# Performance work log

Measured on AMD Instinct MI355X. Metric: run time of the kernel, lower is better.

Reference implementation:

```python
import jax, jax.numpy as jnp
import numpy as np

IN_F = 4096
OUT_F = 4096
B, S = 4, 2048
RMS_EPS = 1e-6
Q_EPS = 1e-5


def setup_inputs() -> dict:
    key = jax.random.key(0)
    kx, kw, kb, ks = jax.random.split(key, 4)
    x = jax.random.normal(kx, (B, S, IN_F), dtype=jnp.float32)
    # ternary BitNet weight in {-1, 0, +1}, stored as float32 for the reference
    W = (jax.random.randint(kw, (OUT_F, IN_F), 0, 3) - 1).astype(jnp.float32)
    rms_weight = jnp.ones((IN_F,), dtype=jnp.float32)
    bias = jax.random.normal(kb, (OUT_F,), dtype=jnp.float32)
    weight_scale = jax.random.uniform(ks, (1,), dtype=jnp.float32) + 0.5
    return {"x": x, "W": W, "rms_weight": rms_weight, "bias": bias,
            "weight_scale": weight_scale}


def reference(x, W, rms_weight, bias, weight_scale):
    # RMSNorm (self.rms_norm applied before quantized matmul)
    var = jnp.mean(x * x, axis=-1, keepdims=True)
    h = x * jax.lax.rsqrt(var + RMS_EPS) * rms_weight
    # BitNet act_quant: per-token absmax int8 quantization
    scale = 127.0 / jnp.clip(jnp.max(jnp.abs(h), axis=-1, keepdims=True), Q_EPS)  # [B,S,1]
    q = jnp.clip(jnp.round(h * scale), -128.0, 127.0)
    # ternary GEMV per token, then dequant
    y = jnp.einsum('bsk,ok->bso', q, W) / scale  # [B,S,OUT_F]
    y = y + bias
    y = y * weight_scale  # weight_scale_mode == 'multiply'
    return y
```

## Files before the change

### kernel.cpp

```cpp
#include <hip/hip_runtime.h>

#define IN_F 4096
#define OUT_F 4096
#define NTOK 8192
#define KDIM 4096

using i32x4 = __attribute__((ext_vector_type(4))) int;
using f32x4 = __attribute__((ext_vector_type(4))) float;

__device__ __forceinline__ void gload_lds16(const void* g, void* l) {
  __builtin_amdgcn_global_load_lds(
      (const __attribute__((address_space(1))) void*)g,
      (__attribute__((address_space(3))) void*)l, 16, 0, 0);
}

#define WAITV(n) asm volatile("s_waitcnt vmcnt(" #n ")" ::: "memory")
#define BAR() do { asm volatile("" ::: "memory"); __builtin_amdgcn_s_barrier(); \
                   asm volatile("" ::: "memory"); } while (0)

__global__ __launch_bounds__(256) void rmsq_kernel(
    const float* __restrict__ x, const float* __restrict__ rmsw,
    signed char* __restrict__ q, float* __restrict__ dscale) {
  const int tok = blockIdx.x;
  const int tid = threadIdx.x;
  const f32x4* xr = (const f32x4*)(x + (size_t)tok * IN_F);
  const f32x4* wr = (const f32x4*)rmsw;

  f32x4 v[4];
  float ss = 0.f;
#pragma unroll
  for (int c = 0; c < 4; ++c) {
    v[c] = xr[c * 256 + tid];
    ss += v[c].x * v[c].x + v[c].y * v[c].y + v[c].z * v[c].z + v[c].w * v[c].w;
  }

  __shared__ float red[4];
#pragma unroll
  for (int off = 32; off > 0; off >>= 1) ss += __shfl_down(ss, off, 64);
  const int wid = tid >> 6;
  if ((tid & 63) == 0) red[wid] = ss;
  __syncthreads();
  const float tot = red[0] + red[1] + red[2] + red[3];
  const float rinv = rsqrtf(tot * (1.0f / IN_F) + 1e-6f);

  f32x4 h[4];
  float amax = 0.f;
#pragma unroll
  for (int c = 0; c < 4; ++c) {
    f32x4 w = wr[c * 256 + tid];
    h[c].x = v[c].x * rinv * w.x;
    h[c].y = v[c].y * rinv * w.y;
    h[c].z = v[c].z * rinv * w.z;
    h[c].w = v[c].w * rinv * w.w;
    amax = fmaxf(amax, fabsf(h[c].x));
    amax = fmaxf(amax, fabsf(h[c].y));
    amax = fmaxf(amax, fabsf(h[c].z));
    amax = fmaxf(amax, fabsf(h[c].w));
  }

  __syncthreads();
#pragma unroll
  for (int off = 32; off > 0; off >>= 1)
    amax = fmaxf(amax, __shfl_down(amax, off, 64));
  if ((tid & 63) == 0) red[wid] = amax;
  __syncthreads();
  amax = fmaxf(fmaxf(red[0], red[1]), fmaxf(red[2], red[3]));
  amax = fmaxf(amax, 1e-5f);
  const float qs = 127.0f / amax;
  if (tid == 0) dscale[tok] = amax * (1.0f / 127.0f);

  uint* qo = (uint*)(q + (size_t)tok * IN_F);
#pragma unroll
  for (int c = 0; c < 4; ++c) {
    float r0 = fminf(fmaxf(rintf(h[c].x * qs), -128.f), 127.f);
    float r1 = fminf(fmaxf(rintf(h[c].y * qs), -128.f), 127.f);
    float r2 = fminf(fmaxf(rintf(h[c].z * qs), -128.f), 127.f);
    float r3 = fminf(fmaxf(rintf(h[c].w * qs), -128.f), 127.f);
    uint p = ((uint)((int)r0 & 255)) | ((uint)((int)r1 & 255) << 8) |
             ((uint)((int)r2 & 255) << 16) | ((uint)((int)r3 & 255) << 24);
    qo[c * 256 + tid] = p;
  }
}

__global__ __launch_bounds__(256) void wconv_kernel(
    const float* __restrict__ W, signed char* __restrict__ Wq) {
  const int idx = blockIdx.x * 256 + threadIdx.x;
  f32x4 w = ((const f32x4*)W)[idx];
  uint p = ((uint)((int)w.x & 255)) | ((uint)((int)w.y & 255) << 8) |
           ((uint)((int)w.z & 255) << 16) | ((uint)((int)w.w & 255) << 24);
  ((uint*)Wq)[idx] = p;
}

#define BM 256
#define BN 256
#define BK 64
#define NT (KDIM / BK)
#define ABYTES (BM * BK)
#define BUFBYTES (2 * ABYTES)

__global__ __launch_bounds__(512, 2) void gemm_kernel(
    const signed char* __restrict__ A, const signed char* __restrict__ Bw,
    const float* __restrict__ dscale, const float* __restrict__ bias,
    const float* __restrict__ wscale_p, float* __restrict__ out) {
  __shared__ __align__(16) signed char lds[3 * BUFBYTES];

  const int tid = threadIdx.x;
  const int lane = tid & 63;
  const int wid = tid >> 6;
  const int wr = wid >> 2;
  const int wc = wid & 3;

  const int bid = blockIdx.x;
  const int swz = (bid & 7) * 64 + (bid >> 3);
  const int m0 = (swz & 31) * BM;
  const int n0 = (swz >> 5) * BN;

  const int cA0 = tid, cA1 = tid + 512;
  const int rA0 = cA0 >> 2, rA1 = cA1 >> 2;
  const int sA0 = (cA0 & 3) ^ ((rA0 >> 1) & 3);
  const int sA1 = (cA1 & 3) ^ ((rA1 >> 1) & 3);
  const signed char* agp0 = A + (size_t)(m0 + rA0) * KDIM + sA0 * 16;
  const signed char* agp1 = A + (size_t)(m0 + rA1) * KDIM + sA1 * 16;
  const signed char* bgp0 = Bw + (size_t)(n0 + rA0) * KDIM + sA0 * 16;
  const signed char* bgp1 = Bw + (size_t)(n0 + rA1) * KDIM + sA1 * 16;

#define STAGE(kt, bufb)                                                    \
  do {                                                                     \
    const int k0_ = (kt) * BK;                                             \
    signed char* lb_ = &lds[(bufb)];                                       \
    gload_lds16(agp0 + k0_, lb_ + cA0 * 16);                               \
    gload_lds16(agp1 + k0_, lb_ + cA1 * 16);                               \
    gload_lds16(bgp0 + k0_, lb_ + ABYTES + cA0 * 16);                      \
    gload_lds16(bgp1 + k0_, lb_ + ABYTES + cA1 * 16);                      \
  } while (0)

  const int fr = lane & 15;
  const int ks = lane >> 4;
  int offA[8], offB[4];
#pragma unroll
  for (int mi = 0; mi < 8; ++mi) {
    const int row = wr * 128 + mi * 16 + fr;
    offA[mi] = row * BK + ((ks ^ ((row >> 1) & 3)) * 16);
  }
#pragma unroll
  for (int ni = 0; ni < 4; ++ni) {
    const int row = wc * 64 + ni * 16 + fr;
    offB[ni] = ABYTES + row * BK + ((ks ^ ((row >> 1) & 3)) * 16);
  }

  i32x4 acc[8][4];
#pragma unroll
  for (int i = 0; i < 8; ++i)
#pragma unroll
    for (int j = 0; j < 4; ++j) acc[i][j] = (i32x4){0, 0, 0, 0};

  STAGE(0, 0);
  STAGE(1, BUFBYTES);
  STAGE(2, 2 * BUFBYTES);

  int bufb = 0;
  for (int t = 0; t < NT; ++t) {
    if (t < NT - 2)       WAITV(8);
    else if (t == NT - 2) WAITV(4);
    else                  WAITV(0);
    BAR();

    const signed char* bp = &lds[bufb];
    i32x4 af[8], bf[4];
#pragma unroll
    for (int mi = 0; mi < 8; ++mi) af[mi] = *(const i32x4*)(bp + offA[mi]);
#pragma unroll
    for (int ni = 0; ni < 4; ++ni) bf[ni] = *(const i32x4*)(bp + offB[ni]);

    __builtin_amdgcn_s_setprio(1);
#pragma unroll
    for (int mi = 0; mi < 8; ++mi)
#pragma unroll
      for (int ni = 0; ni < 4; ++ni)
        acc[mi][ni] = __builtin_amdgcn_mfma_i32_16x16x64_i8(af[mi], bf[ni],
                                                            acc[mi][ni], 0, 0, 0);
    __builtin_amdgcn_s_setprio(0);
    BAR();

    if (t + 3 < NT) STAGE(t + 3, bufb);
    bufb += BUFBYTES;
    if (bufb == 3 * BUFBYTES) bufb = 0;
  }

  const float wsc = wscale_p[0];
  const int rbase = (lane >> 4) * 4;
  float bv[4];
#pragma unroll
  for (int ni = 0; ni < 4; ++ni) bv[ni] = bias[n0 + wc * 64 + ni * 16 + fr];
#pragma unroll
  for (int mi = 0; mi < 8; ++mi) {
#pragma unroll
    for (int r = 0; r < 4; ++r) {
      const int m = m0 + wr * 128 + mi * 16 + rbase + r;
      const float ds = dscale[m];
      float* orow = out + (size_t)m * OUT_F + n0 + wc * 64;
#pragma unroll
      for (int ni = 0; ni < 4; ++ni) {
        orow[ni * 16 + fr] = ((float)acc[mi][ni][r] * ds + bv[ni]) * wsc;
      }
    }
  }
#undef STAGE
}

extern "C" void kernel_launch(void* const* d_in, const int* in_sizes, int n_in,
                              void* d_out, int out_size, void* d_ws, size_t ws_size,
                              hipStream_t stream) {
  const float* x = (const float*)d_in[0];
  const float* W = (const float*)d_in[1];
  const float* rmsw = (const float*)d_in[2];
  const float* bias = (const float*)d_in[3];
  const float* wscale = (const float*)d_in[4];
  float* out = (float*)d_out;

  signed char* q = (signed char*)d_ws;
  signed char* Wq = q + (size_t)NTOK * IN_F;
  float* dscale = (float*)(Wq + (size_t)OUT_F * IN_F);

  rmsq_kernel<<<NTOK, 256, 0, stream>>>(x, rmsw, q, dscale);
  wconv_kernel<<<(OUT_F * IN_F / 4) / 256, 256, 0, stream>>>(W, Wq);
  gemm_kernel<<<(NTOK / BM) * (OUT_F / BN), 512, 0, stream>>>(q, Wq, dscale,
                                                              bias, wscale, out);
}
```

Before: 195.5 us.

## Interleave prefetch loads with quartered MFMA batches using a four-buffer LDS ring

The int8 GEMM main loop is restructured to use four LDS buffers instead of three. Each k-tile is split into four quarters, and each quarter issues one of the four global-to-LDS prefetch loads for tile t+3 between its fragment reads and its MFMA batch. The vmcnt wait moves to the end of the last quarter, so the aim is to spread memory issue evenly across the compute. In exchange, each k-tile now has eight workgroup barriers instead of two, and the LDS footprint grows to 128KB per block.

```diff
diff --git a/kernel.cpp b/kernel.cpp
--- a/kernel.cpp
+++ b/kernel.cpp
@@ -95,14 +95,15 @@
 #define BN 256
 #define BK 64
 #define NT (KDIM / BK)
-#define ABYTES (BM * BK)
-#define BUFBYTES (2 * ABYTES)
+#define TILEB (BM * BK)
+#define BUFB (2 * TILEB)
+#define NBUF 4
 
 __global__ __launch_bounds__(512, 2) void gemm_kernel(
     const signed char* __restrict__ A, const signed char* __restrict__ Bw,
     const float* __restrict__ dscale, const float* __restrict__ bias,
     const float* __restrict__ wscale_p, float* __restrict__ out) {
-  __shared__ __align__(16) signed char lds[3 * BUFBYTES];
+  __shared__ __align__(16) signed char lds[NBUF * BUFB];
 
   const int tid = threadIdx.x;
   const int lane = tid & 63;
@@ -124,14 +125,14 @@
   const signed char* bgp0 = Bw + (size_t)(n0 + rA0) * KDIM + sA0 * 16;
   const signed char* bgp1 = Bw + (size_t)(n0 + rA1) * KDIM + sA1 * 16;
 
-#define STAGE(kt, bufb)                                                    \
+#define STAGE_ALL(kt, bufoff)                                              \
   do {                                                                     \
     const int k0_ = (kt) * BK;                                             \
-    signed char* lb_ = &lds[(bufb)];                                       \
+    signed char* lb_ = &lds[(bufoff)];                                     \
     gload_lds16(agp0 + k0_, lb_ + cA0 * 16);                               \
     gload_lds16(agp1 + k0_, lb_ + cA1 * 16);                               \
-    gload_lds16(bgp0 + k0_, lb_ + ABYTES + cA0 * 16);                      \
-    gload_lds16(bgp1 + k0_, lb_ + ABYTES + cA1 * 16);                      \
+    gload_lds16(bgp0 + k0_, lb_ + TILEB + cA0 * 16);                       \
+    gload_lds16(bgp1 + k0_, lb_ + TILEB + cA1 * 16);                       \
   } while (0)
 
   const int fr = lane & 15;
@@ -145,7 +146,7 @@
 #pragma unroll
   for (int ni = 0; ni < 4; ++ni) {
     const int row = wc * 64 + ni * 16 + fr;
-    offB[ni] = ABYTES + row * BK + ((ks ^ ((row >> 1) & 3)) * 16);
+    offB[ni] = TILEB + row * BK + ((ks ^ ((row >> 1) & 3)) * 16);
   }
 
   i32x4 acc[8][4];
@@ -154,37 +155,61 @@
 #pragma unroll
     for (int j = 0; j < 4; ++j) acc[i][j] = (i32x4){0, 0, 0, 0};
 
-  STAGE(0, 0);
-  STAGE(1, BUFBYTES);
-  STAGE(2, 2 * BUFBYTES);
-
-  int bufb = 0;
+  STAGE_ALL(0, 0);
+  STAGE_ALL(1, BUFB);
+  STAGE_ALL(2, 2 * BUFB);
+  WAITV(8);
+  BAR();
+
+  int bufo = 0;
+  int sbufo = 3 * BUFB;
   for (int t = 0; t < NT; ++t) {
-    if (t < NT - 2)       WAITV(8);
-    else if (t == NT - 2) WAITV(4);
-    else                  WAITV(0);
-    BAR();
-
-    const signed char* bp = &lds[bufb];
-    i32x4 af[8], bf[4];
-#pragma unroll
-    for (int mi = 0; mi < 8; ++mi) af[mi] = *(const i32x4*)(bp + offA[mi]);
-#pragma unroll
-    for (int ni = 0; ni < 4; ++ni) bf[ni] = *(const i32x4*)(bp + offB[ni]);
-
-    __builtin_amdgcn_s_setprio(1);
-#pragma unroll
-    for (int mi = 0; mi < 8; ++mi)
-#pragma unroll
-      for (int ni = 0; ni < 4; ++ni)
-        acc[mi][ni] = __builtin_amdgcn_mfma_i32_16x16x64_i8(af[mi], bf[ni],
-                                                            acc[mi][ni], 0, 0, 0);
-    __builtin_amdgcn_s_setprio(0);
-    BAR();
-
-    if (t + 3 < NT) STAGE(t + 3, bufb);
-    bufb += BUFBYTES;
-    if (bufb == 3 * BUFBYTES) bufb = 0;
+    const signed char* bp = &lds[bufo];
+    signed char* sb = &lds[sbufo];
+    const int k3 = (t + 3) * BK;
+    const bool more = (t + 3 < NT);
+
+#pragma unroll
+    for (int q = 0; q < 4; ++q) {
+      const int mi0 = (q >> 1) * 4;
+      const int ni0 = (q & 1) * 2;
+
+      i32x4 af0 = *(const i32x4*)(bp + offA[mi0 + 0]);
+      i32x4 af1 = *(const i32x4*)(bp + offA[mi0 + 1]);
+      i32x4 af2 = *(const i32x4*)(bp + offA[mi0 + 2]);
+      i32x4 af3 = *(const i32x4*)(bp + offA[mi0 + 3]);
+      i32x4 bf0 = *(const i32x4*)(bp + offB[ni0 + 0]);
+      i32x4 bf1 = *(const i32x4*)(bp + offB[ni0 + 1]);
+
+      if (more) {
+        if (q == 0)      gload_lds16(agp0 + k3, sb + cA0 * 16);
+        else if (q == 1) gload_lds16(agp1 + k3, sb + cA1 * 16);
+        else if (q == 2) gload_lds16(bgp0 + k3, sb + TILEB + cA0 * 16);
+        else             gload_lds16(bgp1 + k3, sb + TILEB + cA1 * 16);
+      }
+
+      BAR();
+      __builtin_amdgcn_s_setprio(1);
+      acc[mi0 + 0][ni0 + 0] = __builtin_amdgcn_mfma_i32_16x16x64_i8(af0, bf0, acc[mi0 + 0][ni0 + 0], 0, 0, 0);
+      acc[mi0 + 1][ni0 + 0] = __builtin_amdgcn_mfma_i32_16x16x64_i8(af1, bf0, acc[mi0 + 1][ni0 + 0], 0, 0, 0);
+      acc[mi0 + 2][ni0 + 0] = __builtin_amdgcn_mfma_i32_16x16x64_i8(af2, bf0, acc[mi0 + 2][ni0 + 0], 0, 0, 0);
+      acc[mi0 + 3][ni0 + 0] = __builtin_amdgcn_mfma_i32_16x16x64_i8(af3, bf0, acc[mi0 + 3][ni0 + 0], 0, 0, 0);
+      acc[mi0 + 0][ni0 + 1] = __builtin_amdgcn_mfma_i32_16x16x64_i8(af0, bf1, acc[mi0 + 0][ni0 + 1], 0, 0, 0);
+      acc[mi0 + 1][ni0 + 1] = __builtin_amdgcn_mfma_i32_16x16x64_i8(af1, bf1, acc[mi0 + 1][ni0 + 1], 0, 0, 0);
+      acc[mi0 + 2][ni0 + 1] = __builtin_amdgcn_mfma_i32_16x16x64_i8(af2, bf1, acc[mi0 + 2][ni0 + 1], 0, 0, 0);
+      acc[mi0 + 3][ni0 + 1] = __builtin_amdgcn_mfma_i32_16x16x64_i8(af3, bf1, acc[mi0 + 3][ni0 + 1], 0, 0, 0);
+      __builtin_amdgcn_s_setprio(0);
+
+      if (q == 3) {
+        if (t < NT - 3)       WAITV(8);
+        else if (t == NT - 3) WAITV(4);
+        else if (t == NT - 2) WAITV(0);
+      }
+      BAR();
+    }
+
+    bufo += BUFB;  if (bufo == NBUF * BUFB) bufo = 0;
+    sbufo += BUFB; if (sbufo == NBUF * BUFB) sbufo = 0;
   }
 
   const float wsc = wscale_p[0];
@@ -205,7 +230,7 @@
       }
     }
   }
-#undef STAGE
+#undef STAGE_ALL
 }
 
 extern "C" void kernel_launch(void* const* d_in, const int* in_sizes, int n_in,
```

Result: slower. 208.6 us (+6.7%).

## Shrink GEMM tile to 128x256 with 4 waves and restructure LDS pipeline

Applied to the files above, without the earlier changes.

Reduces the GEMM block tile from 256x256 with 8 waves to 128x256 with 4 waves, so the grid has twice as many blocks. The triple-buffered LDS pipeline now issues the stage-ahead loads right after the fragment reads and drops the second barrier per iteration, prefetching 2 tiles ahead instead of 3. The aim is better occupancy and load balancing and less barrier overhead. In exchange, operand reuse per block drops (B traffic per A row is higher), and correctness depends on the single barrier being enough to protect buffer reuse.

```diff
diff --git a/kernel.cpp b/kernel.cpp
--- a/kernel.cpp
+++ b/kernel.cpp
@@ -91,47 +91,55 @@
   ((uint*)Wq)[idx] = p;
 }
 
-#define BM 256
+#define BM 128
 #define BN 256
 #define BK 64
 #define NT (KDIM / BK)
-#define ABYTES (BM * BK)
-#define BUFBYTES (2 * ABYTES)
-
-__global__ __launch_bounds__(512, 2) void gemm_kernel(
+#define ATILEB (BM * BK)
+#define BTILEB (BN * BK)
+#define BUFB (ATILEB + BTILEB)
+#define NBUF 3
+
+__global__ __launch_bounds__(256, 2) void gemm_kernel(
     const signed char* __restrict__ A, const signed char* __restrict__ Bw,
     const float* __restrict__ dscale, const float* __restrict__ bias,
     const float* __restrict__ wscale_p, float* __restrict__ out) {
-  __shared__ __align__(16) signed char lds[3 * BUFBYTES];
+  __shared__ __align__(16) signed char lds[NBUF * BUFB];
 
   const int tid = threadIdx.x;
   const int lane = tid & 63;
-  const int wid = tid >> 6;
-  const int wr = wid >> 2;
-  const int wc = wid & 3;
+  const int wc = tid >> 6;
 
   const int bid = blockIdx.x;
-  const int swz = (bid & 7) * 64 + (bid >> 3);
-  const int m0 = (swz & 31) * BM;
-  const int n0 = (swz >> 5) * BN;
-
-  const int cA0 = tid, cA1 = tid + 512;
+  const int swz = (bid & 7) * 128 + (bid >> 3);
+  const int m0 = (swz & 63) * BM;
+  const int n0 = (swz >> 6) * BN;
+
+  const int cA0 = tid, cA1 = tid + 256;
   const int rA0 = cA0 >> 2, rA1 = cA1 >> 2;
   const int sA0 = (cA0 & 3) ^ ((rA0 >> 1) & 3);
   const int sA1 = (cA1 & 3) ^ ((rA1 >> 1) & 3);
   const signed char* agp0 = A + (size_t)(m0 + rA0) * KDIM + sA0 * 16;
   const signed char* agp1 = A + (size_t)(m0 + rA1) * KDIM + sA1 * 16;
-  const signed char* bgp0 = Bw + (size_t)(n0 + rA0) * KDIM + sA0 * 16;
-  const signed char* bgp1 = Bw + (size_t)(n0 + rA1) * KDIM + sA1 * 16;
-
-#define STAGE(kt, bufb)                                                    \
+  const int rB = tid >> 2;
+  const signed char* bgp[4];
+#pragma unroll
+  for (int j = 0; j < 4; ++j) {
+    const int rBj = rB + j * 64;
+    const int sBj = (tid & 3) ^ ((rBj >> 1) & 3);
+    bgp[j] = Bw + (size_t)(n0 + rBj) * KDIM + sBj * 16;
+  }
+
+#define STAGE(kt, boff)                                                    \
   do {                                                                     \
     const int k0_ = (kt) * BK;                                             \
-    signed char* lb_ = &lds[(bufb)];                                       \
+    signed char* lb_ = &lds[(boff)];                                       \
     gload_lds16(agp0 + k0_, lb_ + cA0 * 16);                               \
     gload_lds16(agp1 + k0_, lb_ + cA1 * 16);                               \
-    gload_lds16(bgp0 + k0_, lb_ + ABYTES + cA0 * 16);                      \
-    gload_lds16(bgp1 + k0_, lb_ + ABYTES + cA1 * 16);                      \
+    gload_lds16(bgp[0] + k0_, lb_ + ATILEB + (tid + 0 * 256) * 16);        \
+    gload_lds16(bgp[1] + k0_, lb_ + ATILEB + (tid + 1 * 256) * 16);        \
+    gload_lds16(bgp[2] + k0_, lb_ + ATILEB + (tid + 2 * 256) * 16);        \
+    gload_lds16(bgp[3] + k0_, lb_ + ATILEB + (tid + 3 * 256) * 16);        \
   } while (0)
 
   const int fr = lane & 15;
@@ -139,13 +147,13 @@
   int offA[8], offB[4];
 #pragma unroll
   for (int mi = 0; mi < 8; ++mi) {
-    const int row = wr * 128 + mi * 16 + fr;
+    const int row = mi * 16 + fr;
     offA[mi] = row * BK + ((ks ^ ((row >> 1) & 3)) * 16);
   }
 #pragma unroll
   for (int ni = 0; ni < 4; ++ni) {
     const int row = wc * 64 + ni * 16 + fr;
-    offB[ni] = ABYTES + row * BK + ((ks ^ ((row >> 1) & 3)) * 16);
+    offB[ni] = ATILEB + row * BK + ((ks ^ ((row >> 1) & 3)) * 16);
   }
 
   i32x4 acc[8][4];
@@ -155,22 +163,22 @@
     for (int j = 0; j < 4; ++j) acc[i][j] = (i32x4){0, 0, 0, 0};
 
   STAGE(0, 0);
-  STAGE(1, BUFBYTES);
-  STAGE(2, 2 * BUFBYTES);
-
-  int bufb = 0;
+  STAGE(1, BUFB);
+
+  int br = 0;
+  int bs = 2 * BUFB;
   for (int t = 0; t < NT; ++t) {
-    if (t < NT - 2)       WAITV(8);
-    else if (t == NT - 2) WAITV(4);
-    else                  WAITV(0);
+    if (t < NT - 1) WAITV(6); else WAITV(0);
     BAR();
 
-    const signed char* bp = &lds[bufb];
+    const signed char* bp = &lds[br];
     i32x4 af[8], bf[4];
 #pragma unroll
     for (int mi = 0; mi < 8; ++mi) af[mi] = *(const i32x4*)(bp + offA[mi]);
 #pragma unroll
     for (int ni = 0; ni < 4; ++ni) bf[ni] = *(const i32x4*)(bp + offB[ni]);
+
+    if (t + 2 < NT) STAGE(t + 2, bs);
 
     __builtin_amdgcn_s_setprio(1);
 #pragma unroll
@@ -180,11 +188,9 @@
         acc[mi][ni] = __builtin_amdgcn_mfma_i32_16x16x64_i8(af[mi], bf[ni],
                                                             acc[mi][ni], 0, 0, 0);
     __builtin_amdgcn_s_setprio(0);
-    BAR();
-
-    if (t + 3 < NT) STAGE(t + 3, bufb);
-    bufb += BUFBYTES;
-    if (bufb == 3 * BUFBYTES) bufb = 0;
+
+    br += BUFB; if (br == NBUF * BUFB) br = 0;
+    bs += BUFB; if (bs == NBUF * BUFB) bs = 0;
   }
 
   const float wsc = wscale_p[0];
@@ -196,7 +202,7 @@
   for (int mi = 0; mi < 8; ++mi) {
 #pragma unroll
     for (int r = 0; r < 4; ++r) {
-      const int m = m0 + wr * 128 + mi * 16 + rbase + r;
+      const int m = m0 + mi * 16 + rbase + r;
       const float ds = dscale[m];
       float* orow = out + (size_t)m * OUT_F + n0 + wc * 64;
 #pragma unroll
@@ -224,6 +230,6 @@
 
   rmsq_kernel<<<NTOK, 256, 0, stream>>>(x, rmsw, q, dscale);
   wconv_kernel<<<(OUT_F * IN_F / 4) / 256, 256, 0, stream>>>(W, Wq);
-  gemm_kernel<<<(NTOK / BM) * (OUT_F / BN), 512, 0, stream>>>(q, Wq, dscale,
+  gemm_kernel<<<(NTOK / BM) * (OUT_F / BN), 256, 0, stream>>>(q, Wq, dscale,
                                                               bias, wscale, out);
 }
```

Measured after the change: 192.0 us. Within noise of the previous version (-1.8%).
